# Optimization experiments

Measured on AMD Instinct MI355X. Metric: run time of the kernel, lower is better.

The kernel has to match this reference:

```python
import jax, jax.numpy as jnp
import numpy as np
import math

DIM = 2048
N_HEADS = 16
HEAD_DIM = DIM // N_HEADS
BASE = 10000
B, S = 2, 2048


def rope_cache(seq_len, head_dim, base):
    theta = 1.0 / (base ** (jnp.arange(0, head_dim, 2, dtype=jnp.float32)[: head_dim // 2] / head_dim))
    idx_theta = jnp.arange(seq_len, dtype=jnp.float32)[:, None] * theta[None, :]  # [S, D/2]
    return jnp.cos(idx_theta), jnp.sin(idx_theta)


def apply_rope(x, cos, sin):
    # x: [B, S, H, D]; cos/sin: [S, D/2]; interleaved-pair rotation
    b, s, h, d = x.shape
    xr = x.astype(jnp.float32).reshape(b, s, h, d // 2, 2)
    c = cos[None, :, None, :]
    sn = sin[None, :, None, :]
    x0, x1 = xr[..., 0], xr[..., 1]
    out = jnp.stack([x0 * c - x1 * sn, x1 * c + x0 * sn], axis=-1)
    return out.reshape(b, s, h, d).astype(x.dtype)


def setup_inputs() -> dict:
    key = jax.random.key(0)
    k1, k2, k3, k4, k5 = jax.random.split(key, 5)
    x = jax.random.normal(k1, (B, S, DIM), dtype=jnp.float32)
    # causal mask: True = masked out (strict upper triangle)
    mask = jnp.triu(jnp.ones((S, S), dtype=bool), k=1)[None, None]  # [1,1,S,S]
    scale = 0.02
    wq = jax.random.normal(k2, (DIM, DIM), dtype=jnp.float32) * scale
    wk = jax.random.normal(k3, (DIM, DIM), dtype=jnp.float32) * scale
    wv = jax.random.normal(k4, (DIM, DIM), dtype=jnp.float32) * scale
    wo = jax.random.normal(k5, (DIM, DIM), dtype=jnp.float32) * scale
    return {"x": x, "mask": mask, "wq": wq, "wk": wk, "wv": wv, "wo": wo}


def reference(x, mask, wq, wk, wv, wo):
    b, s, _ = x.shape
    cos, sin = rope_cache(s, HEAD_DIM, BASE)
    q = (x @ wq.T).reshape(b, s, N_HEADS, HEAD_DIM)
    k = (x @ wk.T).reshape(b, s, N_HEADS, HEAD_DIM)
    v = (x @ wv.T).reshape(b, s, N_HEADS, HEAD_DIM)
    q = apply_rope(q, cos, sin)
    k = apply_rope(k, cos, sin)
    # [B, H, S, S]
    scores = jnp.einsum('bqhd,bkhd->bhqk', q, k) / math.sqrt(HEAD_DIM)
    scores = jnp.where(mask, -jnp.inf, scores)
    attn = jax.nn.softmax(scores.astype(jnp.float32), axis=-1).astype(q.dtype)
    out = jnp.einsum('bhqk,bkhd->bqhd', attn, v).reshape(b, s, DIM)
    return out @ wo.T
```

## Files before the change

kernel.cpp:

```cpp
#include <hip/hip_runtime.h>
#include <hip/hip_bf16.h>
#include <math.h>

#define DIM   2048
#define NH    16
#define HD    128
#define SEQ   2048
#define BATCH 2
#define QKVN  6144

typedef __attribute__((ext_vector_type(8))) short short8;
typedef __attribute__((ext_vector_type(4))) float f32x4;
typedef __attribute__((ext_vector_type(4))) unsigned int u32x4;
typedef __attribute__((ext_vector_type(4))) _Float16 half4;

static __device__ __forceinline__ unsigned short f2bf(float f) {
    __hip_bfloat16 h = __float2bfloat16(f);
    return *reinterpret_cast<unsigned short*>(&h);
}

static __device__ __forceinline__ void gload16(const void* g, void* l) {
    __builtin_amdgcn_global_load_lds(
        (const __attribute__((address_space(1))) void*)(g),
        (__attribute__((address_space(3))) void*)(l), 16, 0, 0);
}

__device__ __forceinline__ void storeC_helper(float* C, size_t idx, float v) { C[idx] = v; }
__device__ __forceinline__ void storeC_helper(__hip_bfloat16* C, size_t idx, float v) { C[idx] = __float2bfloat16(v); }

#define GFENCE()  asm volatile("" ::: "memory")
#define GBAR()    do { GFENCE(); __builtin_amdgcn_s_barrier(); GFENCE(); } while (0)
#define GWAITL0() do { asm volatile("s_waitcnt lgkmcnt(0)" ::: "memory"); __builtin_amdgcn_sched_barrier(0); } while (0)
#define GWAITV(n) asm volatile("s_waitcnt vmcnt(" n ")" ::: "memory")

__global__ __launch_bounds__(256) void cast_all(const float* __restrict__ x,
                                                const float* __restrict__ wq,
                                                const float* __restrict__ wk,
                                                const float* __restrict__ wv,
                                                const float* __restrict__ wo,
                                                __hip_bfloat16* __restrict__ xb,
                                                __hip_bfloat16* __restrict__ wqkvb,
                                                __hip_bfloat16* __restrict__ wob) {
    const int VX = (BATCH * SEQ * DIM) / 4;
    const int VW = (DIM * DIM) / 4;
    int v = blockIdx.x * blockDim.x + threadIdx.x;
    const float* src; __hip_bfloat16* dst; int off;
    if (v < VX)               { src = x;  dst = xb;                            off = v; }
    else if (v < VX + VW)     { src = wq; dst = wqkvb;                         off = v - VX; }
    else if (v < VX + 2 * VW) { src = wk; dst = wqkvb + (size_t)DIM * DIM;     off = v - VX - VW; }
    else if (v < VX + 3 * VW) { src = wv; dst = wqkvb + 2ull * DIM * DIM;      off = v - VX - 2 * VW; }
    else                      { src = wo; dst = wob;                           off = v - VX - 3 * VW; }
    float4 f = *(const float4*)(src + (size_t)off * 4);
    union { unsigned short u[4]; uint2 d; } pk;
    pk.u[0] = f2bf(f.x); pk.u[1] = f2bf(f.y); pk.u[2] = f2bf(f.z); pk.u[3] = f2bf(f.w);
    *(uint2*)(dst + (size_t)off * 4) = pk.d;
}

template <int MOFF>
static __device__ __forceinline__ void mfma16(const short8 (&af)[4], const short8 (&bf)[4],
                                              f32x4 (&acc)[8][4]) {
    __builtin_amdgcn_s_setprio(1);
#pragma unroll
    for (int mt = 0; mt < 4; mt++)
#pragma unroll
        for (int nt = 0; nt < 4; nt++)
            acc[MOFF + mt][nt] = __builtin_amdgcn_mfma_f32_16x16x32_bf16(
                af[mt], bf[nt], acc[MOFF + mt][nt], 0, 0, 0);
    __builtin_amdgcn_s_setprio(0);
}

__global__ __attribute__((amdgpu_waves_per_eu(2, 2))) __launch_bounds__(512)
void gemm256_qkv(const __hip_bfloat16* __restrict__ A,
                 const __hip_bfloat16* __restrict__ B,
                 __hip_bfloat16* __restrict__ C,
                 _Float16* __restrict__ vt) {
    constexpr int K  = DIM;
    constexpr int N  = QKVN;
    constexpr int NT = K / 64;
    constexpr int NI = NT / 2;
    __shared__ __align__(16) __hip_bfloat16 As[2][256 * 64];
    __shared__ __align__(16) __hip_bfloat16 Bs[2][256 * 64];

    int tid  = threadIdx.x;
    int lane = tid & 63;
    int wave = tid >> 6;
    int wm   = wave >> 2;
    int wn   = wave & 3;
    int quad = lane >> 4;
    int l15  = lane & 15;
    int m0   = blockIdx.y * 256;
    int n0   = blockIdx.x * 256;

    f32x4 acc[8][4] = {};

    auto stage = [&](int tau, int h) {
        const __hip_bfloat16* src;
        __hip_bfloat16* dst;
        if (h < 2) { src = A + (size_t)(m0 + h * 128) * K + tau * 64;
                     dst = &As[tau & 1][h * 8192]; }
        else       { src = B + (size_t)(n0 + (h - 2) * 128) * K + tau * 64;
                     dst = &Bs[tau & 1][(h - 2) * 8192]; }
#pragma unroll
        for (int c = 0; c < 2; c++) {
            int br = (wave * 2 + c) * 8;
            int r  = br + (lane >> 3);
            int cc = (lane & 7) ^ (r & 7);
            gload16(src + (size_t)r * K + cc * 8, dst + br * 64);
        }
    };

    int swz = l15 & 7;
    const __hip_bfloat16* a00 = &As[0][(wm * 128 + l15) * 64 + ((quad    ) ^ swz) * 8];
    const __hip_bfloat16* a01 = &As[0][(wm * 128 + l15) * 64 + ((4 + quad) ^ swz) * 8];
    const __hip_bfloat16* b00 = &Bs[0][(wn * 64  + l15) * 64 + ((quad    ) ^ swz) * 8];
    const __hip_bfloat16* b01 = &Bs[0][(wn * 64  + l15) * 64 + ((4 + quad) ^ swz) * 8];

    short8 fa[4], fb[4];

    stage(0, 0); stage(0, 1); stage(0, 2); stage(0, 3);
    GWAITV("0");
    GBAR();

#pragma unroll 1
    for (int i = 0; i < NI; i++) {
        const bool nl = (i < NI - 1);
        stage(2 * i + 1, 2); stage(2 * i + 1, 3);
#pragma unroll
        for (int t = 0; t < 4; t++) fa[t] = *(const short8*)(a00 + t * 1024);
#pragma unroll
        for (int t = 0; t < 4; t++) fb[t] = *(const short8*)(b00 + t * 1024);
        GBAR(); GWAITL0(); mfma16<0>(fa, fb, acc); GBAR();
        stage(2 * i + 1, 0);
#pragma unroll
        for (int t = 0; t < 4; t++) fa[t] = *(const short8*)(a00 + (4 + t) * 1024);
        GBAR(); GWAITL0(); mfma16<4>(fa, fb, acc); GBAR();
        stage(2 * i + 1, 1);
#pragma unroll
        for (int t = 0; t < 4; t++) fa[t] = *(const short8*)(a01 + t * 1024);
#pragma unroll
        for (int t = 0; t < 4; t++) fb[t] = *(const short8*)(b01 + t * 1024);
        GBAR(); GWAITL0(); mfma16<0>(fa, fb, acc); GBAR();
#pragma unroll
        for (int t = 0; t < 4; t++) fa[t] = *(const short8*)(a01 + (4 + t) * 1024);
        GBAR(); GWAITL0(); mfma16<4>(fa, fb, acc);
        GWAITV("0");
        GBAR();
        if (nl) { stage(2 * i + 2, 2); stage(2 * i + 2, 3); }
#pragma unroll
        for (int t = 0; t < 4; t++) fa[t] = *(const short8*)(a00 + 16384 + t * 1024);
#pragma unroll
        for (int t = 0; t < 4; t++) fb[t] = *(const short8*)(b00 + 16384 + t * 1024);
        GBAR(); GWAITL0(); mfma16<0>(fa, fb, acc); GBAR();
        if (nl) stage(2 * i + 2, 0);
#pragma unroll
        for (int t = 0; t < 4; t++) fa[t] = *(const short8*)(a00 + 16384 + (4 + t) * 1024);
        GBAR(); GWAITL0(); mfma16<4>(fa, fb, acc); GBAR();
        if (nl) stage(2 * i + 2, 1);
#pragma unroll
        for (int t = 0; t < 4; t++) fa[t] = *(const short8*)(a01 + 16384 + t * 1024);
#pragma unroll
        for (int t = 0; t < 4; t++) fb[t] = *(const short8*)(b01 + 16384 + t * 1024);
        GBAR(); GWAITL0(); mfma16<0>(fa, fb, acc); GBAR();
#pragma unroll
        for (int t = 0; t < 4; t++) fa[t] = *(const short8*)(a01 + 16384 + (4 + t) * 1024);
        GBAR(); GWAITL0(); mfma16<4>(fa, fb, acc);
        if (nl) GWAITV("0");
        GBAR();
    }

    int ncol0 = n0 + wn * 64;
    if (ncol0 >= 4096) {
        _Float16* T = ((wave < 4) ? (_Float16*)As : (_Float16*)Bs) + (wave & 3) * 8192;
#pragma unroll
        for (int mt = 0; mt < 8; mt++)
#pragma unroll
            for (int nt = 0; nt < 4; nt++) {
                half4 hv;
#pragma unroll
                for (int r = 0; r < 4; r++) hv[r] = (_Float16)acc[mt][nt][r];
                int chunk = mt * 2 + (quad >> 1);
                int phys  = chunk ^ l15;
                *(half4*)(T + (nt * 16 + l15) * 128 + phys * 8 + (quad & 1) * 4) = hv;
            }
        int h  = (ncol0 - 4096) >> 7;
        int d0 = (ncol0 - 4096) & 127;
        int b  = (m0 + wm * 128) >> 11;
        int sb = (m0 + wm * 128) & (SEQ - 1);
#pragma unroll
        for (int pass = 0; pass < 16; pass++) {
            int d = pass * 4 + quad;
            int phys = l15 ^ (d & 15);
            u32x4 val = *(const u32x4*)(T + d * 128 + phys * 8);
            *(u32x4*)(vt + ((size_t)((b * NH + h) * HD + d0 + d)) * SEQ + sb + l15 * 8) = val;
        }
    } else {
#pragma unroll
        for (int nt = 0; nt < 4; nt++) {
            int col = ncol0 + nt * 16 + l15;
            float theta = __expf(-((float)((col & 127) & ~1) * (1.0f / (float)HD)) * 9.210340371976184f);
#pragma unroll
            for (int mt = 0; mt < 8; mt++)
#pragma unroll
                for (int r = 0; r < 4; r++) {
                    int row = m0 + wm * 128 + mt * 16 + quad * 4 + r;
                    float val = acc[mt][nt][r];
                    float part = __shfl_xor(val, 1);
                    int s = row & (SEQ - 1);
                    float sn, cs;
                    __sincosf((float)s * theta, &sn, &cs);
                    val = (l15 & 1) ? val * cs + part * sn : val * cs - part * sn;
                    C[(size_t)row * N + col] = __float2bfloat16(val);
                }
        }
    }
}

template <int MODE, typename OutT>
__global__ __launch_bounds__(256) void gemm_bt(const __hip_bfloat16* __restrict__ A,
                                               const __hip_bfloat16* __restrict__ B,
                                               OutT* __restrict__ C,
                                               _Float16* __restrict__ vt,
                                               int M, int N, int K) {
    constexpr int BK = 64;
    __shared__ __align__(16) __hip_bfloat16 As[128 * BK];
    __shared__ __align__(16) __hip_bfloat16 Bs[128 * BK];
    int tid  = threadIdx.x;
    int lane = tid & 63;
    int wave = tid >> 6;
    int quad = lane >> 4;
    int l15  = lane & 15;
    int wr   = wave >> 1, wc = wave & 1;
    int m0 = blockIdx.y * 128;
    int n0 = blockIdx.x * 128;
    f32x4 acc[4][4] = {};

    for (int k0 = 0; k0 < K; k0 += BK) {
        __syncthreads();
#pragma unroll
        for (int c = 0; c < 4; c++) {
            int br = (wave * 4 + c) * 8;
            int r  = br + (lane >> 3);
            int cc = (lane & 7) ^ (r & 7);
            gload16(A + (size_t)(m0 + r) * K + k0 + cc * 8, As + br * 64);
            gload16(B + (size_t)(n0 + r) * K + k0 + cc * 8, Bs + br * 64);
        }
        __syncthreads();
#pragma unroll
        for (int kk = 0; kk < BK; kk += 32) {
            short8 af[4], bf4[4];
#pragma unroll
            for (int t = 0; t < 4; t++) {
                int Ra = wr * 64 + t * 16 + l15;
                int pa = ((kk >> 3) + quad) ^ (Ra & 7);
                af[t] = *(const short8*)(As + Ra * 64 + pa * 8);
                int Rb = wc * 64 + t * 16 + l15;
                int pb = ((kk >> 3) + quad) ^ (Rb & 7);
                bf4[t] = *(const short8*)(Bs + Rb * 64 + pb * 8);
            }
#pragma unroll
            for (int mt = 0; mt < 4; mt++)
#pragma unroll
                for (int nt = 0; nt < 4; nt++)
                    acc[mt][nt] = __builtin_amdgcn_mfma_f32_16x16x32_bf16(af[mt], bf4[nt], acc[mt][nt], 0, 0, 0);
        }
    }

#pragma unroll
    for (int nt = 0; nt < 4; nt++) {
        int col = n0 + wc * 64 + nt * 16 + l15;
#pragma unroll
        for (int mt = 0; mt < 4; mt++)
#pragma unroll
            for (int r = 0; r < 4; r++) {
                int row = m0 + wr * 64 + mt * 16 + quad * 4 + r;
                storeC_helper(C, (size_t)row * N + col, acc[mt][nt][r]);
            }
    }
}

__global__ __launch_bounds__(512, 2) void flash_kernel(const __hip_bfloat16* __restrict__ qkv,
                                                       const _Float16* __restrict__ vt,
                                                       __hip_bfloat16* __restrict__ attn) {
    __shared__ __align__(16) __hip_bfloat16 Ks[2][2][64 * 128];
    __shared__ __align__(16) _Float16 Vts[2][2][128 * 64];
    int tid  = threadIdx.x;
    int lane = tid & 63;
    int wave = tid >> 6;
    int grp  = wave >> 2;
    int wl   = wave & 3;
    int quad = lane >> 4;
    int l15  = lane & 15;
    int pairi = blockIdx.x;
    int bh = blockIdx.y;
    int b  = bh >> 4;
    int h  = bh & 15;
    size_t row0 = (size_t)b * SEQ;
    const _Float16* vbase = vt + (size_t)bh * HD * SEQ;
    const float scale = 0.08838834764831845f;
    const float NEG = -1e30f;

    auto stage = [&](int buf, int kt) {
#pragma unroll
        for (int c = 0; c < 4; c++) {
            int br = (wl * 4 + c) * 4;
            int r  = br + (lane >> 4);
            int cc = (lane & 15) ^ (r & 15);
            gload16(qkv + (row0 + kt * 64 + r) * (size_t)QKVN + DIM + h * HD + cc * 8,
                    &Ks[grp][buf][br * 128]);
        }
#pragma unroll
        for (int c = 0; c < 4; c++) {
            int br = (wl * 4 + c) * 8;
            int r  = br + (lane >> 3);
            int cc = (lane & 7) ^ ((r >> 1) & 7);
            gload16(vbase + (size_t)r * SEQ + kt * 64 + cc * 8, &Vts[grp][buf][br * 64]);
        }
    };

    for (int seg = 0; seg < 2; seg++) {
        int qt = seg ? (15 - pairi) : pairi;
        int half = qt + 1;
        int kbase = grp ? half : 0;

        short8 qf[2][4];
#pragma unroll
        for (int mt = 0; mt < 2; mt++) {
            int qrow = qt * 128 + wl * 32 + mt * 16 + l15;
            const __hip_bfloat16* qptr = qkv + (row0 + qrow) * (size_t)QKVN + h * HD + quad * 8;
#pragma unroll
            for (int c = 0; c < 4; c++) qf[mt][c] = *(const short8*)(qptr + c * 32);
        }
        f32x4 o[2][8] = {};
        float m_[2] = {NEG, NEG}, l_[2] = {0.f, 0.f};

        stage(0, kbase);

        for (int i = 0; i < half; i++) {
            __syncthreads();
            if (i + 1 < half) stage((i + 1) & 1, kbase + i + 1);
            int kt = kbase + i;
            const __hip_bfloat16* ks = Ks[grp][i & 1];
            const _Float16* vts = Vts[grp][i & 1];

            f32x4 s[2][4] = {};
#pragma unroll
            for (int ktile = 0; ktile < 4; ktile++) {
                int R = ktile * 16 + l15;
#pragma unroll
                for (int c = 0; c < 4; c++) {
                    int phys = (c * 4 + quad) ^ (R & 15);
                    short8 kf = *(const short8*)(ks + R * 128 + phys * 8);
                    s[0][ktile] = __builtin_amdgcn_mfma_f32_16x16x32_bf16(kf, qf[0][c], s[0][ktile], 0, 0, 0);
                    s[1][ktile] = __builtin_amdgcn_mfma_f32_16x16x32_bf16(kf, qf[1][c], s[1][ktile], 0, 0, 0);
                }
            }
            bool diag = (kt >= 2 * qt);
            float alpha[2];
#pragma unroll
            for (int mt = 0; mt < 2; mt++) {
                int q = qt * 128 + wl * 32 + mt * 16 + l15;
#pragma unroll
                for (int ktile = 0; ktile < 4; ktile++)
#pragma unroll
                    for (int r = 0; r < 4; r++) {
                        float v = s[mt][ktile][r] * scale;
                        if (diag) {
                            int key = kt * 64 + ktile * 16 + quad * 4 + r;
                            if (key > q) v = NEG;
                        }
                        s[mt][ktile][r] = v;
                    }
                float v = s[mt][0][0];
#pragma unroll
                for (int ktile = 0; ktile < 4; ktile++)
#pragma unroll
                    for (int r = 0; r < 4; r++) v = fmaxf(v, s[mt][ktile][r]);
                v = fmaxf(v, __shfl_xor(v, 16));
                v = fmaxf(v, __shfl_xor(v, 32));
                float mnew = fmaxf(m_[mt], v);
                alpha[mt] = __expf(m_[mt] - mnew);
                m_[mt] = mnew;
                float sum = 0.f;
#pragma unroll
                for (int ktile = 0; ktile < 4; ktile++)
#pragma unroll
                    for (int r = 0; r < 4; r++) {
                        float p = __expf(s[mt][ktile][r] - mnew);
                        s[mt][ktile][r] = p;
                        sum += p;
                    }
                sum += __shfl_xor(sum, 16);
                sum += __shfl_xor(sum, 32);
                l_[mt] = l_[mt] * alpha[mt] + sum;
#pragma unroll
                for (int dt = 0; dt < 8; dt++) o[mt][dt] *= alpha[mt];
            }
            half4 pk[2][4];
#pragma unroll
            for (int mt = 0; mt < 2; mt++)
#pragma unroll
                for (int kc = 0; kc < 4; kc++)
#pragma unroll
                    for (int r = 0; r < 4; r++) pk[mt][kc][r] = (_Float16)s[mt][kc][r];
#pragma unroll
            for (int kc = 0; kc < 4; kc++)
#pragma unroll
                for (int dt = 0; dt < 8; dt++) {
                    int d = dt * 16 + l15;
                    int c4 = ((kc * 4 + quad) ^ (d & 14));
                    half4 vf = *(const half4*)(vts + d * 64 + c4 * 4);
                    o[0][dt] = __builtin_amdgcn_mfma_f32_16x16x16f16(vf, pk[0][kc], o[0][dt], 0, 0, 0);
                    o[1][dt] = __builtin_amdgcn_mfma_f32_16x16x16f16(vf, pk[1][kc], o[1][dt], 0, 0, 0);
                }
        }

        __syncthreads();
        float* o1mb = (float*)&Ks[0][0][0];
        float* mlmb = (float*)&Vts[0][0][0];
        __hip_bfloat16* tb = (__hip_bfloat16*)((char*)&Vts[0][0][0] + 8192);
        if (grp == 1) {
            float* dst = o1mb + wl * 4096;
#pragma unroll
            for (int mt = 0; mt < 2; mt++)
#pragma unroll
                for (int dt = 0; dt < 8; dt++)
#pragma unroll
                    for (int r = 0; r < 4; r++)
                        dst[((mt * 8 + dt) * 4 + r) * 64 + lane] = o[mt][dt][r];
            float* ml = mlmb + (wl * 64 + lane) * 4;
            ml[0] = m_[0]; ml[1] = m_[1]; ml[2] = l_[0]; ml[3] = l_[1];
        }
        __syncthreads();
        if (grp == 0) {
            const float* src = o1mb + wl * 4096;
            const float* ml = mlmb + (wl * 64 + lane) * 4;
#pragma unroll
            for (int mt = 0; mt < 2; mt++) {
                float m1 = ml[mt], l1 = ml[2 + mt];
                float mm = fmaxf(m_[mt], m1);
                float a0 = __expf(m_[mt] - mm), a1 = __expf(m1 - mm);
                float linv = 1.0f / (l_[mt] * a0 + l1 * a1);
#pragma unroll
                for (int dt = 0; dt < 8; dt++)
#pragma unroll
                    for (int r = 0; r < 4; r++)
                        o[mt][dt][r] = (o[mt][dt][r] * a0 +
                                        src[((mt * 8 + dt) * 4 + r) * 64 + lane] * a1) * linv;
            }
            __hip_bfloat16* tw = tb + wl * 4096;
#pragma unroll
            for (int mt = 0; mt < 2; mt++)
#pragma unroll
                for (int dt = 0; dt < 8; dt++) {
                    int q32 = mt * 16 + l15;
                    int c4 = dt * 4 + quad;
                    int phys = c4 ^ ((q32 & 7) << 2);
                    union { unsigned short u[4]; uint2 dw; } pkb;
#pragma unroll
                    for (int r = 0; r < 4; r++) pkb.u[r] = f2bf(o[mt][dt][r]);
                    *(uint2*)(tw + q32 * 128 + phys * 4) = pkb.dw;
                }
#pragma unroll
            for (int pass = 0; pass < 8; pass++) {
                int q32 = pass * 4 + (lane >> 4);
                int p = l15;
                int phys = (p * 2) ^ ((q32 & 7) << 2);
                u32x4 val = *(const u32x4*)(tw + q32 * 128 + phys * 4);
                int qg = qt * 128 + wl * 32 + q32;
                *(u32x4*)(attn + (row0 + qg) * (size_t)DIM + h * HD + p * 8) = val;
            }
        }
        __syncthreads();
    }
}

extern "C" void kernel_launch(void* const* d_in, const int* in_sizes, int n_in,
                              void* d_out, int out_size, void* d_ws, size_t ws_size,
                              hipStream_t stream) {
    const float* x  = (const float*)d_in[0];
    const float* wq = (const float*)d_in[2];
    const float* wk = (const float*)d_in[3];
    const float* wv = (const float*)d_in[4];
    const float* wo = (const float*)d_in[5];
    float* out = (float*)d_out;

    char* ws = (char*)d_ws;
    __hip_bfloat16* xb    = (__hip_bfloat16*)(ws);
    __hip_bfloat16* attn  = (__hip_bfloat16*)(ws);
    __hip_bfloat16* wqkvb = (__hip_bfloat16*)(ws + 16777216ull);
    __hip_bfloat16* wob   = (__hip_bfloat16*)(ws + 41943040ull);
    __hip_bfloat16* qkv   = (__hip_bfloat16*)(ws + 50331648ull);
    _Float16*       vtg   = (_Float16*)(ws + 100663296ull);

    const int nv = (BATCH * SEQ * DIM + 4 * DIM * DIM) / 4;
    cast_all<<<nv / 256, 256, 0, stream>>>(x, wq, wk, wv, wo, xb, wqkvb, wob);

    gemm256_qkv<<<dim3(QKVN / 256, (BATCH * SEQ) / 256), 512, 0, stream>>>(
        xb, wqkvb, qkv, vtg);

    flash_kernel<<<dim3(8, BATCH * NH), 512, 0, stream>>>(qkv, vtg, attn);

    gemm_bt<0, float><<<dim3(DIM / 128, (BATCH * SEQ) / 128), 256, 0, stream>>>(
        attn, wob, out, nullptr, BATCH * SEQ, DIM, DIM);
}
```

Baseline: 414.4 us.

## Restructure QKV GEMM to 4-stage K=32 LDS pipeline with 3-deep prefetch

The QKV projection GEMM main loop switches from a double-buffered K=64 tile scheme to a four-buffer ring of K=32 tiles with three tiles kept in flight via vmcnt-based waits. Swizzling and staging are reworked for 32-wide rows. The aim is to hide global-load latency better and simplify the loop schedule. The trade-off is more barriers per unit of K work and a smaller MFMA batch between synchronizations. LDS usage stays the same.

```diff
diff --git a/kernel.cpp b/kernel.cpp
--- a/kernel.cpp
+++ b/kernel.cpp
@@ -76,10 +76,9 @@
                  _Float16* __restrict__ vt) {
     constexpr int K  = DIM;
     constexpr int N  = QKVN;
-    constexpr int NT = K / 64;
-    constexpr int NI = NT / 2;
-    __shared__ __align__(16) __hip_bfloat16 As[2][256 * 64];
-    __shared__ __align__(16) __hip_bfloat16 Bs[2][256 * 64];
+    constexpr int NT = K / 32;
+    __shared__ __align__(16) __hip_bfloat16 As4[4][256 * 32];
+    __shared__ __align__(16) __hip_bfloat16 Bs4[4][256 * 32];
 
     int tid  = threadIdx.x;
     int lane = tid & 63;
@@ -93,84 +92,56 @@
 
     f32x4 acc[8][4] = {};
 
-    auto stage = [&](int tau, int h) {
-        const __hip_bfloat16* src;
-        __hip_bfloat16* dst;
-        if (h < 2) { src = A + (size_t)(m0 + h * 128) * K + tau * 64;
-                     dst = &As[tau & 1][h * 8192]; }
-        else       { src = B + (size_t)(n0 + (h - 2) * 128) * K + tau * 64;
-                     dst = &Bs[tau & 1][(h - 2) * 8192]; }
-#pragma unroll
-        for (int c = 0; c < 2; c++) {
-            int br = (wave * 2 + c) * 8;
-            int r  = br + (lane >> 3);
-            int cc = (lane & 7) ^ (r & 7);
-            gload16(src + (size_t)r * K + cc * 8, dst + br * 64);
+    auto stage32 = [&](int tau, int j) {
+        int rl = tid >> 2;
+        int ch = (tid & 3) ^ ((rl >> 1) & 3);
+        int rowbase = (j & 1) * 128;
+        if (j < 2) {
+            gload16(A + (size_t)(m0 + rowbase + rl) * K + tau * 32 + ch * 8,
+                    &As4[tau & 3][(rowbase + wave * 16) * 32]);
+        } else {
+            gload16(B + (size_t)(n0 + rowbase + rl) * K + tau * 32 + ch * 8,
+                    &Bs4[tau & 3][(rowbase + wave * 16) * 32]);
         }
     };
 
-    int swz = l15 & 7;
-    const __hip_bfloat16* a00 = &As[0][(wm * 128 + l15) * 64 + ((quad    ) ^ swz) * 8];
-    const __hip_bfloat16* a01 = &As[0][(wm * 128 + l15) * 64 + ((4 + quad) ^ swz) * 8];
-    const __hip_bfloat16* b00 = &Bs[0][(wn * 64  + l15) * 64 + ((quad    ) ^ swz) * 8];
-    const __hip_bfloat16* b01 = &Bs[0][(wn * 64  + l15) * 64 + ((4 + quad) ^ swz) * 8];
-
-    short8 fa[4], fb[4];
-
-    stage(0, 0); stage(0, 1); stage(0, 2); stage(0, 3);
-    GWAITV("0");
+    int chv  = (quad ^ ((l15 >> 1) & 3)) * 8;
+    int aoff = (wm * 128 + l15) * 32 + chv;
+    int boff = (wn * 64 + l15) * 32 + chv;
+
+    for (int t = 0; t < 3; t++)
+        for (int j = 0; j < 4; j++) stage32(t, j);
+    GWAITV("8");
     GBAR();
 
+    short8 fA[4], fB[4];
+
 #pragma unroll 1
-    for (int i = 0; i < NI; i++) {
-        const bool nl = (i < NI - 1);
-        stage(2 * i + 1, 2); stage(2 * i + 1, 3);
-#pragma unroll
-        for (int t = 0; t < 4; t++) fa[t] = *(const short8*)(a00 + t * 1024);
-#pragma unroll
-        for (int t = 0; t < 4; t++) fb[t] = *(const short8*)(b00 + t * 1024);
-        GBAR(); GWAITL0(); mfma16<0>(fa, fb, acc); GBAR();
-        stage(2 * i + 1, 0);
-#pragma unroll
-        for (int t = 0; t < 4; t++) fa[t] = *(const short8*)(a00 + (4 + t) * 1024);
-        GBAR(); GWAITL0(); mfma16<4>(fa, fb, acc); GBAR();
-        stage(2 * i + 1, 1);
-#pragma unroll
-        for (int t = 0; t < 4; t++) fa[t] = *(const short8*)(a01 + t * 1024);
-#pragma unroll
-        for (int t = 0; t < 4; t++) fb[t] = *(const short8*)(b01 + t * 1024);
-        GBAR(); GWAITL0(); mfma16<0>(fa, fb, acc); GBAR();
-#pragma unroll
-        for (int t = 0; t < 4; t++) fa[t] = *(const short8*)(a01 + (4 + t) * 1024);
-        GBAR(); GWAITL0(); mfma16<4>(fa, fb, acc);
-        GWAITV("0");
+    for (int T = 0; T < NT; T++) {
+        const __hip_bfloat16* ab = &As4[T & 3][0];
+        const __hip_bfloat16* bb = &Bs4[T & 3][0];
+        if (T < NT - 3) { stage32(T + 3, 0); stage32(T + 3, 1); }
+#pragma unroll
+        for (int t = 0; t < 4; t++) fB[t] = *(const short8*)(bb + boff + t * 512);
+#pragma unroll
+        for (int t = 0; t < 4; t++) fA[t] = *(const short8*)(ab + aoff + t * 512);
+        GBAR(); GWAITL0();
+        mfma16<0>(fA, fB, acc);
         GBAR();
-        if (nl) { stage(2 * i + 2, 2); stage(2 * i + 2, 3); }
-#pragma unroll
-        for (int t = 0; t < 4; t++) fa[t] = *(const short8*)(a00 + 16384 + t * 1024);
-#pragma unroll
-        for (int t = 0; t < 4; t++) fb[t] = *(const short8*)(b00 + 16384 + t * 1024);
-        GBAR(); GWAITL0(); mfma16<0>(fa, fb, acc); GBAR();
-        if (nl) stage(2 * i + 2, 0);
-#pragma unroll
-        for (int t = 0; t < 4; t++) fa[t] = *(const short8*)(a00 + 16384 + (4 + t) * 1024);
-        GBAR(); GWAITL0(); mfma16<4>(fa, fb, acc); GBAR();
-        if (nl) stage(2 * i + 2, 1);
-#pragma unroll
-        for (int t = 0; t < 4; t++) fa[t] = *(const short8*)(a01 + 16384 + t * 1024);
-#pragma unroll
-        for (int t = 0; t < 4; t++) fb[t] = *(const short8*)(b01 + 16384 + t * 1024);
-        GBAR(); GWAITL0(); mfma16<0>(fa, fb, acc); GBAR();
-#pragma unroll
-        for (int t = 0; t < 4; t++) fa[t] = *(const short8*)(a01 + 16384 + (4 + t) * 1024);
-        GBAR(); GWAITL0(); mfma16<4>(fa, fb, acc);
-        if (nl) GWAITV("0");
+        if (T < NT - 3) { stage32(T + 3, 2); stage32(T + 3, 3); }
+#pragma unroll
+        for (int t = 0; t < 4; t++) fA[t] = *(const short8*)(ab + aoff + (4 + t) * 512);
+        GBAR(); GWAITL0();
+        mfma16<4>(fA, fB, acc);
+        if (T < NT - 3)      { GWAITV("8"); }
+        else if (T == NT - 3) { GWAITV("4"); }
+        else if (T == NT - 2) { GWAITV("0"); }
         GBAR();
     }
 
     int ncol0 = n0 + wn * 64;
     if (ncol0 >= 4096) {
-        _Float16* T = ((wave < 4) ? (_Float16*)As : (_Float16*)Bs) + (wave & 3) * 8192;
+        _Float16* T = ((wave < 4) ? (_Float16*)As4 : (_Float16*)Bs4) + (wave & 3) * 8192;
 #pragma unroll
         for (int mt = 0; mt < 8; mt++)
 #pragma unroll
```

Measured after the change: 427.4 us. 3.1% more time.
